# Kernel tuning notes

Hardware: AMD Instinct MI355X
Metric: run time of the kernel (lower is better)

Reference implementation:

```python
import jax, jax.numpy as jnp
import numpy as np

THRESHOLD = 0.01


def setup_inputs() -> dict:
    key = jax.random.key(0)
    kv_cache = jax.random.normal(key, (2, 16, 8192, 128), dtype=jnp.float32)
    return {"kv_cache": kv_cache}


def _dequantize_bin(kv, binmask, levels):
    # min/max restricted to the bin via +-inf sentinels (no dynamic shapes)
    inf = jnp.float32(jnp.inf)
    bmin = jnp.min(jnp.where(binmask, kv, inf))
    bmax = jnp.max(jnp.where(binmask, kv, -inf))
    has_any = jnp.any(binmask)
    valid = has_any & (bmax != bmin)
    denom = jnp.where(valid, bmax - bmin, jnp.float32(1.0))  # safe denom
    q = jnp.round((kv - bmin) / denom * levels)
    deq = q / levels * denom + bmin
    return jnp.where(binmask & valid, deq, kv)


def reference(kv_cache):
    mask = jnp.abs(kv_cache) > THRESHOLD  # large-value bin
    out = _dequantize_bin(kv_cache, ~mask, jnp.float32(15.0))   # small bin: 4-bit
    out = jnp.where(mask, _dequantize_bin(kv_cache, mask, jnp.float32(255.0)), out)  # large bin: 8-bit
    return out
```

## Files before the change

kernel.cpp:

```cpp
#include <hip/hip_runtime.h>

static constexpr float kThresh = 0.01f;
static constexpr int RBLOCKS = 1024;

__device__ __forceinline__ unsigned fkey(float f) {
    unsigned u = __float_as_uint(f);
    return (u & 0x80000000u) ? ~u : (u | 0x80000000u);
}
__device__ __forceinline__ float unkey(unsigned k) {
    unsigned u = (k & 0x80000000u) ? (k & 0x7fffffffu) : ~k;
    return __uint_as_float(u);
}

__device__ __forceinline__ void acc_one(float x, unsigned& smin, unsigned& smax,
                                        unsigned& lmin, unsigned& lmax) {
    unsigned k = fkey(x);
    if (fabsf(x) > kThresh) {
        lmin = min(lmin, k);
        lmax = max(lmax, k);
    } else {
        smin = min(smin, k);
        smax = max(smax, k);
    }
}

__device__ __forceinline__ void wave_reduce4(unsigned& smin, unsigned& smax,
                                             unsigned& lmin, unsigned& lmax) {
    #pragma unroll
    for (int off = 32; off > 0; off >>= 1) {
        smin = min(smin, (unsigned)__shfl_down((int)smin, off));
        smax = max(smax, (unsigned)__shfl_down((int)smax, off));
        lmin = min(lmin, (unsigned)__shfl_down((int)lmin, off));
        lmax = max(lmax, (unsigned)__shfl_down((int)lmax, off));
    }
}

__global__ __launch_bounds__(256) void kv_partial(const float* __restrict__ in, int n,
                                                  unsigned* __restrict__ partials) {
    unsigned smin = 0xFFFFFFFFu, smax = 0u, lmin = 0xFFFFFFFFu, lmax = 0u;
    const int n4 = n >> 2;
    const float4* __restrict__ in4 = (const float4*)in;
    const int stride = gridDim.x * blockDim.x;
    for (int i = blockIdx.x * blockDim.x + threadIdx.x; i < n4; i += stride) {
        float4 v = in4[i];
        acc_one(v.x, smin, smax, lmin, lmax);
        acc_one(v.y, smin, smax, lmin, lmax);
        acc_one(v.z, smin, smax, lmin, lmax);
        acc_one(v.w, smin, smax, lmin, lmax);
    }
    for (int i = (n4 << 2) + blockIdx.x * blockDim.x + threadIdx.x; i < n; i += stride) {
        acc_one(in[i], smin, smax, lmin, lmax);
    }

    wave_reduce4(smin, smax, lmin, lmax);

    __shared__ unsigned ls[4][4];
    const int wave = threadIdx.x >> 6;
    if ((threadIdx.x & 63) == 0) {
        ls[wave][0] = smin; ls[wave][1] = smax; ls[wave][2] = lmin; ls[wave][3] = lmax;
    }
    __syncthreads();
    if (threadIdx.x == 0) {
        unsigned a = ls[0][0], b = ls[0][1], c = ls[0][2], d = ls[0][3];
        #pragma unroll
        for (int w = 1; w < 4; ++w) {
            a = min(a, ls[w][0]); b = max(b, ls[w][1]);
            c = min(c, ls[w][2]); d = max(d, ls[w][3]);
        }
        partials[blockIdx.x * 4 + 0] = a;
        partials[blockIdx.x * 4 + 1] = b;
        partials[blockIdx.x * 4 + 2] = c;
        partials[blockIdx.x * 4 + 3] = d;
    }
}

__global__ __launch_bounds__(256) void kv_final(const unsigned* __restrict__ partials,
                                                unsigned* __restrict__ ws) {
    unsigned smin = 0xFFFFFFFFu, smax = 0u, lmin = 0xFFFFFFFFu, lmax = 0u;
    for (int i = threadIdx.x; i < RBLOCKS; i += 256) {
        smin = min(smin, partials[4 * i + 0]);
        smax = max(smax, partials[4 * i + 1]);
        lmin = min(lmin, partials[4 * i + 2]);
        lmax = max(lmax, partials[4 * i + 3]);
    }
    wave_reduce4(smin, smax, lmin, lmax);

    __shared__ unsigned ls[4][4];
    const int wave = threadIdx.x >> 6;
    if ((threadIdx.x & 63) == 0) {
        ls[wave][0] = smin; ls[wave][1] = smax; ls[wave][2] = lmin; ls[wave][3] = lmax;
    }
    __syncthreads();
    if (threadIdx.x == 0) {
        unsigned a = ls[0][0], b = ls[0][1], c = ls[0][2], d = ls[0][3];
        #pragma unroll
        for (int w = 1; w < 4; ++w) {
            a = min(a, ls[w][0]); b = max(b, ls[w][1]);
            c = min(c, ls[w][2]); d = max(d, ls[w][3]);
        }
        ws[0] = a; ws[1] = b; ws[2] = c; ws[3] = d;
    }
}

__device__ __forceinline__ float deq1(float x, float smin, float ssc, float sis, bool sv,
                                      float lmin, float lsc, float lis, bool lv) {
    bool large = fabsf(x) > kThresh;
    float bmin = large ? lmin : smin;
    float sc   = large ? lsc : ssc;
    float is   = large ? lis : sis;
    bool  v    = large ? lv : sv;
    float q = rintf((x - bmin) * sc);
    float d = fmaf(q, is, bmin);
    return v ? d : x;
}

__global__ __launch_bounds__(256) void kv_dequant(const float* __restrict__ in,
                                                  float* __restrict__ out, int n,
                                                  const unsigned* __restrict__ ws) {
    const unsigned sk0 = ws[0], sk1 = ws[1], lk0 = ws[2], lk1 = ws[3];
    const bool sv = sk0 < sk1;
    const bool lv = lk0 < lk1;
    const float smin = unkey(sk0);
    const float sden = sv ? (unkey(sk1) - smin) : 1.0f;
    const float lmin = unkey(lk0);
    const float lden = lv ? (unkey(lk1) - lmin) : 1.0f;
    const float ssc = 15.0f / sden,  sis = sden / 15.0f;
    const float lsc = 255.0f / lden, lis = lden / 255.0f;

    const int n4 = n >> 2;
    const int i = blockIdx.x * blockDim.x + threadIdx.x;
    const float4* __restrict__ in4 = (const float4*)in;
    float4* __restrict__ out4 = (float4*)out;
    if (i < n4) {
        float4 v = in4[i];
        float4 r;
        r.x = deq1(v.x, smin, ssc, sis, sv, lmin, lsc, lis, lv);
        r.y = deq1(v.y, smin, ssc, sis, sv, lmin, lsc, lis, lv);
        r.z = deq1(v.z, smin, ssc, sis, sv, lmin, lsc, lis, lv);
        r.w = deq1(v.w, smin, ssc, sis, sv, lmin, lsc, lis, lv);
        out4[i] = r;
    }
    const int tail = n - (n4 << 2);
    if (i < tail) {
        int j = (n4 << 2) + i;
        out[j] = deq1(in[j], smin, ssc, sis, sv, lmin, lsc, lis, lv);
    }
}

extern "C" void kernel_launch(void* const* d_in, const int* in_sizes, int n_in,
                              void* d_out, int out_size, void* d_ws, size_t ws_size,
                              hipStream_t stream) {
    const float* in = (const float*)d_in[0];
    float* out = (float*)d_out;
    unsigned* ws = (unsigned*)d_ws;
    const int n = in_sizes[0];

    unsigned* partials = (unsigned*)d_out;

    kv_partial<<<RBLOCKS, 256, 0, stream>>>(in, n, partials);
    kv_final<<<1, 256, 0, stream>>>(partials, ws);

    const int n4 = n >> 2;
    int dblocks = (n4 + 255) / 256;
    if (dblocks < 1) dblocks = 1;
    kv_dequant<<<dblocks, 256, 0, stream>>>(in, out, n, ws);
}
```

Measured before the change: 245.0 us.

## Fuse reduction and dequantization into one cooperative persistent kernel

Replaces the three-kernel pipeline (partial reduce, final reduce, dequant) with a single cooperative kernel that uses grid-wide syncs. Every block redundantly reduces the partials to get the bin parameters, then dequantizes with 2x unrolled loads and nontemporal stores. This removes the extra launch gaps and the single-block final kernel. It depends on cooperative launch support, keeps the old path as a fallback, and adds the cost of two grid barriers.

```diff
diff --git a/kernel.cpp b/kernel.cpp
--- a/kernel.cpp
+++ b/kernel.cpp
@@ -1,7 +1,14 @@
 #include <hip/hip_runtime.h>
+#include <hip/hip_cooperative_groups.h>
+
+namespace cg = cooperative_groups;
 
 static constexpr float kThresh = 0.01f;
+static constexpr int TPB     = 256;
+static constexpr int NBLK    = 1024;
 static constexpr int RBLOCKS = 1024;
+
+typedef float f32x4 __attribute__((ext_vector_type(4)));
 
 __device__ __forceinline__ unsigned fkey(float f) {
     unsigned u = __float_as_uint(f);
@@ -24,6 +31,14 @@
     }
 }
 
+__device__ __forceinline__ void acc4(float4 v, unsigned& smin, unsigned& smax,
+                                     unsigned& lmin, unsigned& lmax) {
+    acc_one(v.x, smin, smax, lmin, lmax);
+    acc_one(v.y, smin, smax, lmin, lmax);
+    acc_one(v.z, smin, smax, lmin, lmax);
+    acc_one(v.w, smin, smax, lmin, lmax);
+}
+
 __device__ __forceinline__ void wave_reduce4(unsigned& smin, unsigned& smax,
                                              unsigned& lmin, unsigned& lmax) {
     #pragma unroll
@@ -32,73 +47,6 @@
         smax = max(smax, (unsigned)__shfl_down((int)smax, off));
         lmin = min(lmin, (unsigned)__shfl_down((int)lmin, off));
         lmax = max(lmax, (unsigned)__shfl_down((int)lmax, off));
-    }
-}
-
-__global__ __launch_bounds__(256) void kv_partial(const float* __restrict__ in, int n,
-                                                  unsigned* __restrict__ partials) {
-    unsigned smin = 0xFFFFFFFFu, smax = 0u, lmin = 0xFFFFFFFFu, lmax = 0u;
-    const int n4 = n >> 2;
-    const float4* __restrict__ in4 = (const float4*)in;
-    const int stride = gridDim.x * blockDim.x;
-    for (int i = blockIdx.x * blockDim.x + threadIdx.x; i < n4; i += stride) {
-        float4 v = in4[i];
-        acc_one(v.x, smin, smax, lmin, lmax);
-        acc_one(v.y, smin, smax, lmin, lmax);
-        acc_one(v.z, smin, smax, lmin, lmax);
-        acc_one(v.w, smin, smax, lmin, lmax);
-    }
-    for (int i = (n4 << 2) + blockIdx.x * blockDim.x + threadIdx.x; i < n; i += stride) {
-        acc_one(in[i], smin, smax, lmin, lmax);
-    }
-
-    wave_reduce4(smin, smax, lmin, lmax);
-
-    __shared__ unsigned ls[4][4];
-    const int wave = threadIdx.x >> 6;
-    if ((threadIdx.x & 63) == 0) {
-        ls[wave][0] = smin; ls[wave][1] = smax; ls[wave][2] = lmin; ls[wave][3] = lmax;
-    }
-    __syncthreads();
-    if (threadIdx.x == 0) {
-        unsigned a = ls[0][0], b = ls[0][1], c = ls[0][2], d = ls[0][3];
-        #pragma unroll
-        for (int w = 1; w < 4; ++w) {
-            a = min(a, ls[w][0]); b = max(b, ls[w][1]);
-            c = min(c, ls[w][2]); d = max(d, ls[w][3]);
-        }
-        partials[blockIdx.x * 4 + 0] = a;
-        partials[blockIdx.x * 4 + 1] = b;
-        partials[blockIdx.x * 4 + 2] = c;
-        partials[blockIdx.x * 4 + 3] = d;
-    }
-}
-
-__global__ __launch_bounds__(256) void kv_final(const unsigned* __restrict__ partials,
-                                                unsigned* __restrict__ ws) {
-    unsigned smin = 0xFFFFFFFFu, smax = 0u, lmin = 0xFFFFFFFFu, lmax = 0u;
-    for (int i = threadIdx.x; i < RBLOCKS; i += 256) {
-        smin = min(smin, partials[4 * i + 0]);
-        smax = max(smax, partials[4 * i + 1]);
-        lmin = min(lmin, partials[4 * i + 2]);
-        lmax = max(lmax, partials[4 * i + 3]);
-    }
-    wave_reduce4(smin, smax, lmin, lmax);
-
-    __shared__ unsigned ls[4][4];
-    const int wave = threadIdx.x >> 6;
-    if ((threadIdx.x & 63) == 0) {
-        ls[wave][0] = smin; ls[wave][1] = smax; ls[wave][2] = lmin; ls[wave][3] = lmax;
-    }
-    __syncthreads();
-    if (threadIdx.x == 0) {
-        unsigned a = ls[0][0], b = ls[0][1], c = ls[0][2], d = ls[0][3];
-        #pragma unroll
-        for (int w = 1; w < 4; ++w) {
-            a = min(a, ls[w][0]); b = max(b, ls[w][1]);
-            c = min(c, ls[w][2]); d = max(d, ls[w][3]);
-        }
-        ws[0] = a; ws[1] = b; ws[2] = c; ws[3] = d;
     }
 }
 
@@ -112,6 +60,180 @@
     float q = rintf((x - bmin) * sc);
     float d = fmaf(q, is, bmin);
     return v ? d : x;
+}
+
+__global__ __launch_bounds__(TPB, 4) void kv_fused(const float* __restrict__ in,
+                                                   float* __restrict__ out, int n,
+                                                   unsigned* __restrict__ pt) {
+    const int n4 = n >> 2;
+    const float4* __restrict__ in4 = (const float4*)in;
+    const int tid = blockIdx.x * TPB + threadIdx.x;
+    const int stride = NBLK * TPB;
+
+    unsigned smin = 0xFFFFFFFFu, smax = 0u, lmin = 0xFFFFFFFFu, lmax = 0u;
+    int i = tid;
+    for (; i + stride < n4; i += 2 * stride) {
+        float4 a = in4[i];
+        float4 b = in4[i + stride];
+        acc4(a, smin, smax, lmin, lmax);
+        acc4(b, smin, smax, lmin, lmax);
+    }
+    for (; i < n4; i += stride) acc4(in4[i], smin, smax, lmin, lmax);
+    for (int j = (n4 << 2) + tid; j < n; j += stride)
+        acc_one(in[j], smin, smax, lmin, lmax);
+
+    wave_reduce4(smin, smax, lmin, lmax);
+
+    __shared__ unsigned ls[4][4];
+    __shared__ float sc8[8];
+    const int wave = threadIdx.x >> 6;
+    if ((threadIdx.x & 63) == 0) {
+        ls[wave][0] = smin; ls[wave][1] = smax; ls[wave][2] = lmin; ls[wave][3] = lmax;
+    }
+    __syncthreads();
+    if (threadIdx.x == 0) {
+        unsigned a = ls[0][0], b = ls[0][1], c = ls[0][2], d = ls[0][3];
+        #pragma unroll
+        for (int w = 1; w < 4; ++w) {
+            a = min(a, ls[w][0]); b = max(b, ls[w][1]);
+            c = min(c, ls[w][2]); d = max(d, ls[w][3]);
+        }
+        __hip_atomic_store(&pt[blockIdx.x * 4 + 0], a, __ATOMIC_RELAXED, __HIP_MEMORY_SCOPE_AGENT);
+        __hip_atomic_store(&pt[blockIdx.x * 4 + 1], b, __ATOMIC_RELAXED, __HIP_MEMORY_SCOPE_AGENT);
+        __hip_atomic_store(&pt[blockIdx.x * 4 + 2], c, __ATOMIC_RELAXED, __HIP_MEMORY_SCOPE_AGENT);
+        __hip_atomic_store(&pt[blockIdx.x * 4 + 3], d, __ATOMIC_RELAXED, __HIP_MEMORY_SCOPE_AGENT);
+    }
+
+    cg::this_grid().sync();
+
+    unsigned fa = 0xFFFFFFFFu, fb = 0u, fc = 0xFFFFFFFFu, fd = 0u;
+    for (int p = threadIdx.x; p < NBLK; p += TPB) {
+        fa = min(fa, __hip_atomic_load(&pt[4 * p + 0], __ATOMIC_RELAXED, __HIP_MEMORY_SCOPE_AGENT));
+        fb = max(fb, __hip_atomic_load(&pt[4 * p + 1], __ATOMIC_RELAXED, __HIP_MEMORY_SCOPE_AGENT));
+        fc = min(fc, __hip_atomic_load(&pt[4 * p + 2], __ATOMIC_RELAXED, __HIP_MEMORY_SCOPE_AGENT));
+        fd = max(fd, __hip_atomic_load(&pt[4 * p + 3], __ATOMIC_RELAXED, __HIP_MEMORY_SCOPE_AGENT));
+    }
+    wave_reduce4(fa, fb, fc, fd);
+    if ((threadIdx.x & 63) == 0) {
+        ls[wave][0] = fa; ls[wave][1] = fb; ls[wave][2] = fc; ls[wave][3] = fd;
+    }
+    __syncthreads();
+    if (threadIdx.x == 0) {
+        unsigned a = ls[0][0], b = ls[0][1], c = ls[0][2], d = ls[0][3];
+        #pragma unroll
+        for (int w = 1; w < 4; ++w) {
+            a = min(a, ls[w][0]); b = max(b, ls[w][1]);
+            c = min(c, ls[w][2]); d = max(d, ls[w][3]);
+        }
+        bool sv = a < b;
+        bool lv = c < d;
+        float smn  = unkey(a);
+        float sden = sv ? (unkey(b) - smn) : 1.0f;
+        float lmn  = unkey(c);
+        float lden = lv ? (unkey(d) - lmn) : 1.0f;
+        sc8[0] = smn; sc8[1] = 15.0f / sden;  sc8[2] = sden / 15.0f;
+        sc8[3] = lmn; sc8[4] = 255.0f / lden; sc8[5] = lden / 255.0f;
+        sc8[6] = sv ? 1.0f : 0.0f;
+        sc8[7] = lv ? 1.0f : 0.0f;
+    }
+    __syncthreads();
+    const float smn = sc8[0], ssc = sc8[1], sis = sc8[2];
+    const float lmn = sc8[3], lsc = sc8[4], lis = sc8[5];
+    const bool  sv  = sc8[6] != 0.0f, lv = sc8[7] != 0.0f;
+
+    cg::this_grid().sync();
+
+    float4* __restrict__ out4 = (float4*)out;
+    int k = tid;
+    for (; k + stride < n4; k += 2 * stride) {
+        float4 a = in4[k];
+        float4 b = in4[k + stride];
+        f32x4 ra, rb;
+        ra.x = deq1(a.x, smn, ssc, sis, sv, lmn, lsc, lis, lv);
+        ra.y = deq1(a.y, smn, ssc, sis, sv, lmn, lsc, lis, lv);
+        ra.z = deq1(a.z, smn, ssc, sis, sv, lmn, lsc, lis, lv);
+        ra.w = deq1(a.w, smn, ssc, sis, sv, lmn, lsc, lis, lv);
+        rb.x = deq1(b.x, smn, ssc, sis, sv, lmn, lsc, lis, lv);
+        rb.y = deq1(b.y, smn, ssc, sis, sv, lmn, lsc, lis, lv);
+        rb.z = deq1(b.z, smn, ssc, sis, sv, lmn, lsc, lis, lv);
+        rb.w = deq1(b.w, smn, ssc, sis, sv, lmn, lsc, lis, lv);
+        __builtin_nontemporal_store(ra, (f32x4*)&out4[k]);
+        __builtin_nontemporal_store(rb, (f32x4*)&out4[k + stride]);
+    }
+    for (; k < n4; k += stride) {
+        float4 a = in4[k];
+        f32x4 r;
+        r.x = deq1(a.x, smn, ssc, sis, sv, lmn, lsc, lis, lv);
+        r.y = deq1(a.y, smn, ssc, sis, sv, lmn, lsc, lis, lv);
+        r.z = deq1(a.z, smn, ssc, sis, sv, lmn, lsc, lis, lv);
+        r.w = deq1(a.w, smn, ssc, sis, sv, lmn, lsc, lis, lv);
+        __builtin_nontemporal_store(r, (f32x4*)&out4[k]);
+    }
+    for (int j = (n4 << 2) + tid; j < n; j += stride)
+        out[j] = deq1(in[j], smn, ssc, sis, sv, lmn, lsc, lis, lv);
+}
+
+__global__ __launch_bounds__(256) void kv_partial(const float* __restrict__ in, int n,
+                                                  unsigned* __restrict__ partials) {
+    unsigned smin = 0xFFFFFFFFu, smax = 0u, lmin = 0xFFFFFFFFu, lmax = 0u;
+    const int n4 = n >> 2;
+    const float4* __restrict__ in4 = (const float4*)in;
+    const int stride = gridDim.x * blockDim.x;
+    for (int i = blockIdx.x * blockDim.x + threadIdx.x; i < n4; i += stride) {
+        float4 v = in4[i];
+        acc4(v, smin, smax, lmin, lmax);
+    }
+    for (int i = (n4 << 2) + blockIdx.x * blockDim.x + threadIdx.x; i < n; i += stride) {
+        acc_one(in[i], smin, smax, lmin, lmax);
+    }
+    wave_reduce4(smin, smax, lmin, lmax);
+
+    __shared__ unsigned ls[4][4];
+    const int wave = threadIdx.x >> 6;
+    if ((threadIdx.x & 63) == 0) {
+        ls[wave][0] = smin; ls[wave][1] = smax; ls[wave][2] = lmin; ls[wave][3] = lmax;
+    }
+    __syncthreads();
+    if (threadIdx.x == 0) {
+        unsigned a = ls[0][0], b = ls[0][1], c = ls[0][2], d = ls[0][3];
+        #pragma unroll
+        for (int w = 1; w < 4; ++w) {
+            a = min(a, ls[w][0]); b = max(b, ls[w][1]);
+            c = min(c, ls[w][2]); d = max(d, ls[w][3]);
+        }
+        partials[blockIdx.x * 4 + 0] = a;
+        partials[blockIdx.x * 4 + 1] = b;
+        partials[blockIdx.x * 4 + 2] = c;
+        partials[blockIdx.x * 4 + 3] = d;
+    }
+}
+
+__global__ __launch_bounds__(256) void kv_final(const unsigned* __restrict__ partials,
+                                                unsigned* __restrict__ ws) {
+    unsigned smin = 0xFFFFFFFFu, smax = 0u, lmin = 0xFFFFFFFFu, lmax = 0u;
+    for (int i = threadIdx.x; i < RBLOCKS; i += 256) {
+        smin = min(smin, partials[4 * i + 0]);
+        smax = max(smax, partials[4 * i + 1]);
+        lmin = min(lmin, partials[4 * i + 2]);
+        lmax = max(lmax, partials[4 * i + 3]);
+    }
+    wave_reduce4(smin, smax, lmin, lmax);
+
+    __shared__ unsigned ls[4][4];
+    const int wave = threadIdx.x >> 6;
+    if ((threadIdx.x & 63) == 0) {
+        ls[wave][0] = smin; ls[wave][1] = smax; ls[wave][2] = lmin; ls[wave][3] = lmax;
+    }
+    __syncthreads();
+    if (threadIdx.x == 0) {
+        unsigned a = ls[0][0], b = ls[0][1], c = ls[0][2], d = ls[0][3];
+        #pragma unroll
+        for (int w = 1; w < 4; ++w) {
+            a = min(a, ls[w][0]); b = max(b, ls[w][1]);
+            c = min(c, ls[w][2]); d = max(d, ls[w][3]);
+        }
+        ws[0] = a; ws[1] = b; ws[2] = c; ws[3] = d;
+    }
 }
 
 __global__ __launch_bounds__(256) void kv_dequant(const float* __restrict__ in,
@@ -155,13 +277,18 @@
     unsigned* ws = (unsigned*)d_ws;
     const int n = in_sizes[0];
 
-    unsigned* partials = (unsigned*)d_out;
-
-    kv_partial<<<RBLOCKS, 256, 0, stream>>>(in, n, partials);
-    kv_final<<<1, 256, 0, stream>>>(partials, ws);
-
-    const int n4 = n >> 2;
-    int dblocks = (n4 + 255) / 256;
-    if (dblocks < 1) dblocks = 1;
-    kv_dequant<<<dblocks, 256, 0, stream>>>(in, out, n, ws);
-}
+    unsigned* pt = (unsigned*)d_out;
+
+    void* args[] = { (void*)&in, (void*)&out, (void*)&n, (void*)&pt };
+    hipError_t err = hipLaunchCooperativeKernel((void*)kv_fused, dim3(NBLK), dim3(TPB),
+                                                args, 0, stream);
+    if (err != hipSuccess) {
+        (void)hipGetLastError();
+        kv_partial<<<RBLOCKS, 256, 0, stream>>>(in, n, pt);
+        kv_final<<<1, 256, 0, stream>>>(pt, ws);
+        const int n4 = n >> 2;
+        int dblocks = (n4 + 255) / 256;
+        if (dblocks < 1) dblocks = 1;
+        kv_dequant<<<dblocks, 256, 0, stream>>>(in, out, n, ws);
+    }
+}
```

New measurement: 491.0 us. +100.4%, slower.

## Replace two-stage min/max reduction with atomic merge and unroll loads

Applied to the files above, without the earlier changes.

The separate final-reduction kernel is replaced by device-wide atomicMin on four workspace words, with the max keys stored bit-inverted so they can also use atomicMin. The workspace is initialised with a memset. The partial-reduction loop is unrolled four ways so each thread has four float4 loads in flight, and the dequant kernel handles two float4 per thread. This removes one kernel launch and the partials round trip, at the cost of a memset launch and some atomic contention.

```diff
diff --git a/kernel.cpp b/kernel.cpp
--- a/kernel.cpp
+++ b/kernel.cpp
@@ -1,7 +1,9 @@
 #include <hip/hip_runtime.h>
 
 static constexpr float kThresh = 0.01f;
-static constexpr int RBLOCKS = 1024;
+static constexpr int TPB     = 256;
+static constexpr int PBLOCKS = 1024;
+static constexpr int FBLOCKS = 2048;
 
 __device__ __forceinline__ unsigned fkey(float f) {
     unsigned u = __float_as_uint(f);
@@ -24,6 +26,14 @@
     }
 }
 
+__device__ __forceinline__ void acc4(float4 v, unsigned& smin, unsigned& smax,
+                                     unsigned& lmin, unsigned& lmax) {
+    acc_one(v.x, smin, smax, lmin, lmax);
+    acc_one(v.y, smin, smax, lmin, lmax);
+    acc_one(v.z, smin, smax, lmin, lmax);
+    acc_one(v.w, smin, smax, lmin, lmax);
+}
+
 __device__ __forceinline__ void wave_reduce4(unsigned& smin, unsigned& smax,
                                              unsigned& lmin, unsigned& lmax) {
     #pragma unroll
@@ -35,22 +45,127 @@
     }
 }
 
-__global__ __launch_bounds__(256) void kv_partial(const float* __restrict__ in, int n,
+__device__ __forceinline__ float deq1(float x, float smin, float ssc, float sis, bool sv,
+                                      float lmin, float lsc, float lis, bool lv) {
+    bool large = fabsf(x) > kThresh;
+    float bmin = large ? lmin : smin;
+    float sc   = large ? lsc : ssc;
+    float is   = large ? lis : sis;
+    bool  v    = large ? lv : sv;
+    float q = rintf((x - bmin) * sc);
+    float d = fmaf(q, is, bmin);
+    return v ? d : x;
+}
+
+__global__ __launch_bounds__(TPB) void kv_partial_atomic(const float* __restrict__ in, int n,
+                                                         unsigned* __restrict__ ws) {
+    unsigned smin = 0xFFFFFFFFu, smax = 0u, lmin = 0xFFFFFFFFu, lmax = 0u;
+    const int n4 = n >> 2;
+    const float4* __restrict__ in4 = (const float4*)in;
+    const int stride = gridDim.x * TPB;
+    int i = blockIdx.x * TPB + threadIdx.x;
+    for (; i + 3 * stride < n4; i += 4 * stride) {
+        float4 a = in4[i];
+        float4 b = in4[i + stride];
+        float4 c = in4[i + 2 * stride];
+        float4 d = in4[i + 3 * stride];
+        acc4(a, smin, smax, lmin, lmax);
+        acc4(b, smin, smax, lmin, lmax);
+        acc4(c, smin, smax, lmin, lmax);
+        acc4(d, smin, smax, lmin, lmax);
+    }
+    for (; i < n4; i += stride) acc4(in4[i], smin, smax, lmin, lmax);
+    for (int j = (n4 << 2) + blockIdx.x * TPB + threadIdx.x; j < n; j += stride)
+        acc_one(in[j], smin, smax, lmin, lmax);
+
+    wave_reduce4(smin, smax, lmin, lmax);
+
+    __shared__ unsigned ls[4][4];
+    const int wave = threadIdx.x >> 6;
+    if ((threadIdx.x & 63) == 0) {
+        ls[wave][0] = smin; ls[wave][1] = smax; ls[wave][2] = lmin; ls[wave][3] = lmax;
+    }
+    __syncthreads();
+    if (threadIdx.x == 0) {
+        unsigned a = ls[0][0], b = ls[0][1], c = ls[0][2], d = ls[0][3];
+        #pragma unroll
+        for (int w = 1; w < 4; ++w) {
+            a = min(a, ls[w][0]); b = max(b, ls[w][1]);
+            c = min(c, ls[w][2]); d = max(d, ls[w][3]);
+        }
+        atomicMin(&ws[0], a);
+        atomicMin(&ws[1], c);
+        atomicMin(&ws[2], ~b);
+        atomicMin(&ws[3], ~d);
+    }
+}
+
+__global__ __launch_bounds__(TPB) void kv_dequant_os(const float* __restrict__ in,
+                                                     float* __restrict__ out, int n,
+                                                     const unsigned* __restrict__ ws) {
+    const unsigned sk0 = ws[0], lk0 = ws[1];
+    const unsigned sk1 = ~ws[2], lk1 = ~ws[3];
+    const bool sv = sk0 < sk1;
+    const bool lv = lk0 < lk1;
+    const float smin = unkey(sk0);
+    const float sden = sv ? (unkey(sk1) - smin) : 1.0f;
+    const float lmin = unkey(lk0);
+    const float lden = lv ? (unkey(lk1) - lmin) : 1.0f;
+    const float ssc = 15.0f / sden,  sis = sden / 15.0f;
+    const float lsc = 255.0f / lden, lis = lden / 255.0f;
+
+    const int n4 = n >> 2;
+    const int T  = gridDim.x * TPB;
+    const int k  = blockIdx.x * TPB + threadIdx.x;
+    const float4* __restrict__ in4 = (const float4*)in;
+    float4* __restrict__ out4 = (float4*)out;
+
+    if (k < n4) {
+        float4 a = in4[k];
+        float4 r;
+        r.x = deq1(a.x, smin, ssc, sis, sv, lmin, lsc, lis, lv);
+        r.y = deq1(a.y, smin, ssc, sis, sv, lmin, lsc, lis, lv);
+        r.z = deq1(a.z, smin, ssc, sis, sv, lmin, lsc, lis, lv);
+        r.w = deq1(a.w, smin, ssc, sis, sv, lmin, lsc, lis, lv);
+        out4[k] = r;
+    }
+    const int k2 = k + T;
+    if (k2 < n4) {
+        float4 a = in4[k2];
+        float4 r;
+        r.x = deq1(a.x, smin, ssc, sis, sv, lmin, lsc, lis, lv);
+        r.y = deq1(a.y, smin, ssc, sis, sv, lmin, lsc, lis, lv);
+        r.z = deq1(a.z, smin, ssc, sis, sv, lmin, lsc, lis, lv);
+        r.w = deq1(a.w, smin, ssc, sis, sv, lmin, lsc, lis, lv);
+        out4[k2] = r;
+    }
+    const int tail = n - (n4 << 2);
+    if (k < tail) {
+        int j = (n4 << 2) + k;
+        out[j] = deq1(in[j], smin, ssc, sis, sv, lmin, lsc, lis, lv);
+    }
+}
+
+__global__ __launch_bounds__(TPB) void kv_partial(const float* __restrict__ in, int n,
                                                   unsigned* __restrict__ partials) {
     unsigned smin = 0xFFFFFFFFu, smax = 0u, lmin = 0xFFFFFFFFu, lmax = 0u;
     const int n4 = n >> 2;
     const float4* __restrict__ in4 = (const float4*)in;
-    const int stride = gridDim.x * blockDim.x;
-    for (int i = blockIdx.x * blockDim.x + threadIdx.x; i < n4; i += stride) {
-        float4 v = in4[i];
-        acc_one(v.x, smin, smax, lmin, lmax);
-        acc_one(v.y, smin, smax, lmin, lmax);
-        acc_one(v.z, smin, smax, lmin, lmax);
-        acc_one(v.w, smin, smax, lmin, lmax);
-    }
-    for (int i = (n4 << 2) + blockIdx.x * blockDim.x + threadIdx.x; i < n; i += stride) {
-        acc_one(in[i], smin, smax, lmin, lmax);
-    }
+    const int stride = gridDim.x * TPB;
+    int i = blockIdx.x * TPB + threadIdx.x;
+    for (; i + 3 * stride < n4; i += 4 * stride) {
+        float4 a = in4[i];
+        float4 b = in4[i + stride];
+        float4 c = in4[i + 2 * stride];
+        float4 d = in4[i + 3 * stride];
+        acc4(a, smin, smax, lmin, lmax);
+        acc4(b, smin, smax, lmin, lmax);
+        acc4(c, smin, smax, lmin, lmax);
+        acc4(d, smin, smax, lmin, lmax);
+    }
+    for (; i < n4; i += stride) acc4(in4[i], smin, smax, lmin, lmax);
+    for (int j = (n4 << 2) + blockIdx.x * TPB + threadIdx.x; j < n; j += stride)
+        acc_one(in[j], smin, smax, lmin, lmax);
 
     wave_reduce4(smin, smax, lmin, lmax);
 
@@ -74,10 +189,10 @@
     }
 }
 
-__global__ __launch_bounds__(256) void kv_final(const unsigned* __restrict__ partials,
+__global__ __launch_bounds__(TPB) void kv_final(const unsigned* __restrict__ partials,
                                                 unsigned* __restrict__ ws) {
     unsigned smin = 0xFFFFFFFFu, smax = 0u, lmin = 0xFFFFFFFFu, lmax = 0u;
-    for (int i = threadIdx.x; i < RBLOCKS; i += 256) {
+    for (int i = threadIdx.x; i < FBLOCKS; i += TPB) {
         smin = min(smin, partials[4 * i + 0]);
         smax = max(smax, partials[4 * i + 1]);
         lmin = min(lmin, partials[4 * i + 2]);
@@ -98,52 +213,7 @@
             a = min(a, ls[w][0]); b = max(b, ls[w][1]);
             c = min(c, ls[w][2]); d = max(d, ls[w][3]);
         }
-        ws[0] = a; ws[1] = b; ws[2] = c; ws[3] = d;
-    }
-}
-
-__device__ __forceinline__ float deq1(float x, float smin, float ssc, float sis, bool sv,
-                                      float lmin, float lsc, float lis, bool lv) {
-    bool large = fabsf(x) > kThresh;
-    float bmin = large ? lmin : smin;
-    float sc   = large ? lsc : ssc;
-    float is   = large ? lis : sis;
-    bool  v    = large ? lv : sv;
-    float q = rintf((x - bmin) * sc);
-    float d = fmaf(q, is, bmin);
-    return v ? d : x;
-}
-
-__global__ __launch_bounds__(256) void kv_dequant(const float* __restrict__ in,
-                                                  float* __restrict__ out, int n,
-                                                  const unsigned* __restrict__ ws) {
-    const unsigned sk0 = ws[0], sk1 = ws[1], lk0 = ws[2], lk1 = ws[3];
-    const bool sv = sk0 < sk1;
-    const bool lv = lk0 < lk1;
-    const float smin = unkey(sk0);
-    const float sden = sv ? (unkey(sk1) - smin) : 1.0f;
-    const float lmin = unkey(lk0);
-    const float lden = lv ? (unkey(lk1) - lmin) : 1.0f;
-    const float ssc = 15.0f / sden,  sis = sden / 15.0f;
-    const float lsc = 255.0f / lden, lis = lden / 255.0f;
-
-    const int n4 = n >> 2;
-    const int i = blockIdx.x * blockDim.x + threadIdx.x;
-    const float4* __restrict__ in4 = (const float4*)in;
-    float4* __restrict__ out4 = (float4*)out;
-    if (i < n4) {
-        float4 v = in4[i];
-        float4 r;
-        r.x = deq1(v.x, smin, ssc, sis, sv, lmin, lsc, lis, lv);
-        r.y = deq1(v.y, smin, ssc, sis, sv, lmin, lsc, lis, lv);
-        r.z = deq1(v.z, smin, ssc, sis, sv, lmin, lsc, lis, lv);
-        r.w = deq1(v.w, smin, ssc, sis, sv, lmin, lsc, lis, lv);
-        out4[i] = r;
-    }
-    const int tail = n - (n4 << 2);
-    if (i < tail) {
-        int j = (n4 << 2) + i;
-        out[j] = deq1(in[j], smin, ssc, sis, sv, lmin, lsc, lis, lv);
+        ws[0] = a; ws[1] = c; ws[2] = ~b; ws[3] = ~d;
     }
 }
 
@@ -155,13 +225,19 @@
     unsigned* ws = (unsigned*)d_ws;
     const int n = in_sizes[0];
 
-    unsigned* partials = (unsigned*)d_out;
-
-    kv_partial<<<RBLOCKS, 256, 0, stream>>>(in, n, partials);
-    kv_final<<<1, 256, 0, stream>>>(partials, ws);
-
-    const int n4 = n >> 2;
-    int dblocks = (n4 + 255) / 256;
+    const int n4 = n >> 2;
+    int dblocks = (n4 + 2 * TPB - 1) / (2 * TPB);
     if (dblocks < 1) dblocks = 1;
-    kv_dequant<<<dblocks, 256, 0, stream>>>(in, out, n, ws);
-}
+
+    if (ws_size >= 4 * sizeof(unsigned)) {
+        hipMemsetAsync(ws, 0xFF, 4 * sizeof(unsigned), stream);
+        kv_partial_atomic<<<PBLOCKS, TPB, 0, stream>>>(in, n, ws);
+        kv_dequant_os<<<dblocks, TPB, 0, stream>>>(in, out, n, ws);
+    } else {
+        unsigned* pt = (unsigned*)d_out;
+        unsigned* w4 = (unsigned*)d_ws;
+        kv_partial<<<FBLOCKS, TPB, 0, stream>>>(in, n, pt);
+        kv_final<<<1, TPB, 0, stream>>>(pt, w4);
+        kv_dequant_os<<<dblocks, TPB, 0, stream>>>(in, out, n, w4);
+    }
+}
```

Result: slower. 280.2 us (+14.4%).
